# Performance work log

Measured on AMD Instinct MI355X. Metric: run time of the kernel, lower is better.

Reference implementation:

```python
import jax, jax.numpy as jnp
import numpy as np

B, T, C = 1, 2048, 2048
H, KH, HD = 16, 4, 128  # n_head, n_kv_head, head_dim
ROPE_BASE = 10000.0


def setup_inputs() -> dict:
    key = jax.random.key(0)
    ks = jax.random.split(key, 5)
    s = 0.02
    return {
        "x": jax.random.normal(ks[0], (B, T, C), jnp.float32),
        "Wq": jax.random.normal(ks[1], (C, H * HD), jnp.float32) * s,
        "Wk": jax.random.normal(ks[2], (C, KH * HD), jnp.float32) * s,
        "Wv": jax.random.normal(ks[3], (C, KH * HD), jnp.float32) * s,
        "Wo": jax.random.normal(ks[4], (H * HD, C), jnp.float32) * s,
        "position_ids": jnp.arange(T, dtype=jnp.int32),
    }


def _rotate_half(a):
    h = a.shape[-1] // 2
    return jnp.concatenate([-a[..., h:], a[..., :h]], axis=-1)


def reference(x, Wq, Wk, Wv, Wo, position_ids):
    b, t, c = x.shape
    n_rep = H // KH
    # projections -> [B, heads, T, HD]
    q = (x @ Wq).reshape(b, t, H, HD).transpose(0, 2, 1, 3)
    k = (x @ Wk).reshape(b, t, KH, HD).transpose(0, 2, 1, 3)
    v = (x @ Wv).reshape(b, t, KH, HD).transpose(0, 2, 1, 3)
    # rotary embedding cache [T, HD]
    inv_freq = 1.0 / (ROPE_BASE ** (jnp.arange(0, HD, 2, dtype=jnp.float32) / HD))
    pos = jnp.arange(t, dtype=jnp.float32)
    freqs = pos[:, None] * inv_freq[None, :]
    emb = jnp.concatenate([freqs, freqs], axis=-1)
    cos = jnp.cos(emb)[position_ids][None, None]  # [1,1,T,HD]
    sin = jnp.sin(emb)[position_ids][None, None]
    q = q * cos + _rotate_half(q) * sin
    k = k * cos + _rotate_half(k) * sin
    # GQA: group query heads instead of materializing repeated K/V
    qg = q.reshape(b, KH, n_rep, t, HD)
    scale = jnp.float32(1.0 / np.sqrt(HD))
    scores = jnp.einsum('bgrtd,bgsd->bgrts', qg, k) * scale
    causal = jnp.tril(jnp.ones((t, t), dtype=bool))
    scores = jnp.where(causal, scores, jnp.float32(-1e30))
    p = jax.nn.softmax(scores, axis=-1)
    y = jnp.einsum('bgrts,bgsd->bgrtd', p, v)
    y = y.reshape(b, H, t, HD).transpose(0, 2, 1, 3).reshape(b, t, H * HD)
    return y @ Wo
```

## Files before the change

kernel.cpp:

```cpp
#include <hip/hip_runtime.h>

typedef unsigned short u16;
using bf16x8 = __attribute__((ext_vector_type(8))) short;
using f32x4  = __attribute__((ext_vector_type(4))) float;

#define GLD16(g, l)                                                            \
  __builtin_amdgcn_global_load_lds(                                            \
      (const __attribute__((address_space(1))) void*)(g),                      \
      (__attribute__((address_space(3))) void*)(l), 16, 0, 0)

__device__ __forceinline__ u16 f2b(float x) {
  union { float f; unsigned u; } v; v.f = x;
  unsigned r = v.u + 0x7FFF + ((v.u >> 16) & 1);
  return (u16)(r >> 16);
}

__global__ void cast_bf16_kernel(const float* __restrict__ in,
                                 u16* __restrict__ out, int n4) {
  int i = blockIdx.x * blockDim.x + threadIdx.x;
  int stride = gridDim.x * blockDim.x;
  for (; i < n4; i += stride) {
    float4 v = ((const float4*)in)[i];
    ushort4 o;
    o.x = f2b(v.x); o.y = f2b(v.y); o.z = f2b(v.z); o.w = f2b(v.w);
    ((ushort4*)out)[i] = o;
  }
}

__global__ void transpose_w_kernel(const float* __restrict__ src,
                                   u16* __restrict__ dst, int K, int N) {
  __shared__ float tile[32][33];
  int n0 = blockIdx.x * 32, k0 = blockIdx.y * 32;
  int tx = threadIdx.x, ty = threadIdx.y;
#pragma unroll
  for (int r = 0; r < 4; r++)
    tile[ty + r * 8][tx] = src[(size_t)(k0 + ty + r * 8) * N + n0 + tx];
  __syncthreads();
#pragma unroll
  for (int r = 0; r < 4; r++)
    dst[(size_t)(n0 + ty + r * 8) * K + k0 + tx] = f2b(tile[tx][ty + r * 8]);
}

__global__ void transpose_v_kernel(const u16* __restrict__ src,
                                   u16* __restrict__ dst) {
  __shared__ u16 tile[32][33];
  int h = blockIdx.z;
  int t0 = blockIdx.x * 32, d0 = blockIdx.y * 32;
  const u16* s = src + (size_t)h * 2048 * 128;
  u16* d = dst + (size_t)h * 128 * 2048;
  int tx = threadIdx.x, ty = threadIdx.y;
#pragma unroll
  for (int r = 0; r < 4; r++)
    tile[ty + r * 8][tx] = s[(size_t)(t0 + ty + r * 8) * 128 + d0 + tx];
  __syncthreads();
#pragma unroll
  for (int r = 0; r < 4; r++)
    d[(size_t)(d0 + ty + r * 8) * 2048 + t0 + tx] = tile[tx][ty + r * 8];
}

__global__ __launch_bounds__(256, 2)
void gemm_bt_128(const u16* __restrict__ A, const u16* __restrict__ Bt,
                 float* __restrict__ C, int M, int N, int K) {
  __shared__ u16 As[128 * 32];
  __shared__ u16 Bs[128 * 32];
  const int tid = threadIdx.x;
  const int lane = tid & 63;
  const int w = tid >> 6;
  const int wr = w >> 1, wc = w & 1;
  const int m0 = blockIdx.y * 128, n0 = blockIdx.x * 128;

  f32x4 acc[4][4] = {};

  const int srow = tid >> 2, skg = tid & 3;
  const u16* Ag0 = A + (size_t)(m0 + srow) * K + skg * 8;
  const u16* Ag1 = A + (size_t)(m0 + 64 + srow) * K + skg * 8;
  const u16* Bg0 = Bt + (size_t)(n0 + srow) * K + skg * 8;
  const u16* Bg1 = Bt + (size_t)(n0 + 64 + srow) * K + skg * 8;
  u16* Al0 = As + tid * 8;
  u16* Al1 = As + (256 + tid) * 8;
  u16* Bl0 = Bs + tid * 8;
  u16* Bl1 = Bs + (256 + tid) * 8;

  const int frow = lane & 15, fk = (lane >> 4) * 8;

  for (int k0 = 0; k0 < K; k0 += 32) {
    GLD16(Ag0 + k0, Al0);
    GLD16(Ag1 + k0, Al1);
    GLD16(Bg0 + k0, Bl0);
    GLD16(Bg1 + k0, Bl1);
    __syncthreads();
    bf16x8 av[4], bv[4];
#pragma unroll
    for (int m = 0; m < 4; m++)
      av[m] = *(const bf16x8*)(As + (wr * 64 + m * 16 + frow) * 32 + fk);
#pragma unroll
    for (int n = 0; n < 4; n++)
      bv[n] = *(const bf16x8*)(Bs + (wc * 64 + n * 16 + frow) * 32 + fk);
#pragma unroll
    for (int m = 0; m < 4; m++)
#pragma unroll
      for (int n = 0; n < 4; n++)
        acc[m][n] =
            __builtin_amdgcn_mfma_f32_16x16x32_bf16(av[m], bv[n], acc[m][n], 0, 0, 0);
    __syncthreads();
  }

  const int crow = (lane >> 4) * 4, ccol = lane & 15;
#pragma unroll
  for (int m = 0; m < 4; m++)
#pragma unroll
    for (int n = 0; n < 4; n++)
#pragma unroll
      for (int r = 0; r < 4; r++)
        C[(size_t)(m0 + wr * 64 + m * 16 + crow + r) * N +
          (n0 + wc * 64 + n * 16 + ccol)] = acc[m][n][r];
}

__global__ void rope_kernel(const float* __restrict__ QKV,
                            const int* __restrict__ pos, u16* __restrict__ Qb,
                            u16* __restrict__ Kb, u16* __restrict__ Vb) {
  const int t = blockIdx.x, tid = threadIdx.x;
  const float p = (float)pos[t];
  const float* row = QKV + (size_t)t * 3072;
  const float qscale = 0.08838834764831845f;
  const float c0 = -0.015625f * 13.287712379549449f;
#pragma unroll
  for (int i = 0; i < 4; i++) {
    int idx = tid + i * 256;
    int head = idx >> 6, d = idx & 63;
    float inv = exp2f((float)d * c0);
    float ang = p * inv;
    float s = sinf(ang), c = cosf(ang);
    float a0 = row[head * 128 + d], a1 = row[head * 128 + d + 64];
    Qb[((size_t)head * 2048 + t) * 128 + d] = f2b((a0 * c - a1 * s) * qscale);
    Qb[((size_t)head * 2048 + t) * 128 + d + 64] = f2b((a1 * c + a0 * s) * qscale);
  }
  {
    int head = tid >> 6, d = tid & 63;
    float inv = exp2f((float)d * c0);
    float ang = p * inv;
    float s = sinf(ang), c = cosf(ang);
    float a0 = row[2048 + head * 128 + d], a1 = row[2048 + head * 128 + d + 64];
    Kb[((size_t)head * 2048 + t) * 128 + d] = f2b(a0 * c - a1 * s);
    Kb[((size_t)head * 2048 + t) * 128 + d + 64] = f2b(a1 * c + a0 * s);
  }
#pragma unroll
  for (int i = 0; i < 2; i++) {
    int e = tid + i * 256;
    int kh = e >> 7, d = e & 127;
    Vb[((size_t)kh * 2048 + t) * 128 + d] = f2b(row[2560 + e]);
  }
}

__global__ __launch_bounds__(256, 2)
void attn_kernel(const u16* __restrict__ Qb, const u16* __restrict__ Kb,
                 const u16* __restrict__ Vtb, u16* __restrict__ Y) {
  __shared__ u16 Ks[2][64 * 128];
  __shared__ u16 Vs[2][128 * 64];
  __shared__ u16 Ps[4][16 * 64];
  const int tid = threadIdx.x, lane = tid & 63, w = tid >> 6;
  const int h = blockIdx.y, g = h >> 2;
  const int q0 = blockIdx.x * 64;
  const int qw = q0 + w * 16;
  const int frow = lane & 15, fgrp = lane >> 4;

  const u16* Kg = Kb + (size_t)g * 2048 * 128;
  const u16* Vg = Vtb + (size_t)g * 128 * 2048;

  bf16x8 qf[4];
  const u16* Qrow = Qb + ((size_t)h * 2048 + (qw + frow)) * 128 + fgrp * 8;
#pragma unroll
  for (int kf = 0; kf < 4; kf++) qf[kf] = *(const bf16x8*)(Qrow + kf * 32);

  f32x4 o[8] = {};
  float mrow[4], lrow[4];
#pragma unroll
  for (int r = 0; r < 4; r++) { mrow[r] = -1e30f; lrow[r] = 0.f; }

  const int njt = q0 / 64 + 1;

#pragma unroll
  for (int i = 0; i < 4; i++) {
    int p = tid + i * 256;
    int kr = p >> 4, kc = (p & 15) ^ (kr & 7);
    GLD16(Kg + (size_t)kr * 128 + kc * 8, &Ks[0][p * 8]);
    int vr = p >> 3, vc = (p & 7) ^ (vr & 7);
    GLD16(Vg + (size_t)vr * 2048 + vc * 8, &Vs[0][p * 8]);
  }
  __syncthreads();

  for (int jt = 0; jt < njt; jt++) {
    const int buf = jt & 1;
    if (jt + 1 < njt) {
      const int j0n = (jt + 1) * 64;
#pragma unroll
      for (int i = 0; i < 4; i++) {
        int p = tid + i * 256;
        int kr = p >> 4, kc = (p & 15) ^ (kr & 7);
        GLD16(Kg + (size_t)(j0n + kr) * 128 + kc * 8, &Ks[buf ^ 1][p * 8]);
        int vr = p >> 3, vc = (p & 7) ^ (vr & 7);
        GLD16(Vg + (size_t)vr * 2048 + j0n + vc * 8, &Vs[buf ^ 1][p * 8]);
      }
    }
    f32x4 sc[4] = {};
#pragma unroll
    for (int c = 0; c < 4; c++)
#pragma unroll
      for (int kf = 0; kf < 4; kf++) {
        int row = c * 16 + frow;
        bf16x8 kv = *(const bf16x8*)(
            &Ks[buf][row * 128 + ((kf * 4 + fgrp) ^ (row & 7)) * 8]);
        sc[c] = __builtin_amdgcn_mfma_f32_16x16x32_bf16(qf[kf], kv, sc[c], 0, 0, 0);
      }
    if (jt == njt - 1) {
      const int j0 = jt * 64;
#pragma unroll
      for (int c = 0; c < 4; c++) {
        int j = j0 + c * 16 + frow;
#pragma unroll
        for (int r = 0; r < 4; r++)
          if (j > qw + fgrp * 4 + r) sc[c][r] = -1e30f;
      }
    }
    float pm[4];
#pragma unroll
    for (int r = 0; r < 4; r++)
      pm[r] = fmaxf(fmaxf(sc[0][r], sc[1][r]), fmaxf(sc[2][r], sc[3][r]));
#pragma unroll
    for (int off = 1; off < 16; off <<= 1)
#pragma unroll
      for (int r = 0; r < 4; r++) pm[r] = fmaxf(pm[r], __shfl_xor(pm[r], off, 64));
    float alpha[4], rs[4];
#pragma unroll
    for (int r = 0; r < 4; r++) {
      float mn = fmaxf(mrow[r], pm[r]);
      alpha[r] = __expf(mrow[r] - mn);
      mrow[r] = mn;
      float s = 0.f;
#pragma unroll
      for (int c = 0; c < 4; c++) { sc[c][r] = __expf(sc[c][r] - mn); s += sc[c][r]; }
      rs[r] = s;
    }
#pragma unroll
    for (int off = 1; off < 16; off <<= 1)
#pragma unroll
      for (int r = 0; r < 4; r++) rs[r] += __shfl_xor(rs[r], off, 64);
#pragma unroll
    for (int r = 0; r < 4; r++) lrow[r] = lrow[r] * alpha[r] + rs[r];
#pragma unroll
    for (int db = 0; db < 8; db++)
#pragma unroll
      for (int r = 0; r < 4; r++) o[db][r] *= alpha[r];
    u16* Pw = Ps[w];
#pragma unroll
    for (int c = 0; c < 4; c++)
#pragma unroll
      for (int r = 0; r < 4; r++) {
        int row = fgrp * 4 + r, col = c * 16 + frow;
        Pw[row * 64 + (((col >> 3) ^ row) & 7) * 8 + (col & 7)] = f2b(sc[c][r]);
      }
    asm volatile("s_waitcnt lgkmcnt(0)" ::: "memory");
    bf16x8 pf[2];
#pragma unroll
    for (int ks = 0; ks < 2; ks++)
      pf[ks] = *(const bf16x8*)(
          &Pw[frow * 64 + ((ks * 4 + fgrp) ^ (frow & 7)) * 8]);
#pragma unroll
    for (int db = 0; db < 8; db++)
#pragma unroll
      for (int ks = 0; ks < 2; ks++) {
        int row = db * 16 + frow;
        bf16x8 vf = *(const bf16x8*)(
            &Vs[buf][row * 64 + ((ks * 4 + fgrp) ^ (row & 7)) * 8]);
        o[db] = __builtin_amdgcn_mfma_f32_16x16x32_bf16(pf[ks], vf, o[db], 0, 0, 0);
      }
    __syncthreads();
  }
#pragma unroll
  for (int r = 0; r < 4; r++) {
    float inv = 1.0f / lrow[r];
    int t = qw + fgrp * 4 + r;
#pragma unroll
    for (int db = 0; db < 8; db++)
      Y[(size_t)t * 2048 + h * 128 + db * 16 + frow] = f2b(o[db][r] * inv);
  }
}

extern "C" void kernel_launch(void* const* d_in, const int* in_sizes, int n_in,
                              void* d_out, int out_size, void* d_ws,
                              size_t ws_size, hipStream_t stream) {
  const float* x  = (const float*)d_in[0];
  const float* Wq = (const float*)d_in[1];
  const float* Wk = (const float*)d_in[2];
  const float* Wv = (const float*)d_in[3];
  const float* Wo = (const float*)d_in[4];
  const int* pos  = (const int*)d_in[5];
  float* out = (float*)d_out;
  char* ws = (char*)d_ws;

  u16* xb      = (u16*)(ws + 0);
  u16* Wqkv_bt = (u16*)(ws + 8388608);
  u16* Wo_bt   = (u16*)(ws + 20971520);
  float* QKV   = (float*)(ws + 29360128);
  u16* Yb      = (u16*)(ws + 29360128);
  u16* Qb      = (u16*)(ws + 54525952);
  u16* Kb      = (u16*)(ws + 62914560);
  u16* Vb      = (u16*)(ws + 65011712);
  u16* Vtb     = (u16*)(ws + 67108864);

  cast_bf16_kernel<<<1024, 256, 0, stream>>>(x, xb, 2048 * 2048 / 4);
  transpose_w_kernel<<<dim3(64, 64), dim3(32, 8), 0, stream>>>(Wq, Wqkv_bt, 2048, 2048);
  transpose_w_kernel<<<dim3(16, 64), dim3(32, 8), 0, stream>>>(Wk, Wqkv_bt + (size_t)2048 * 2048, 2048, 512);
  transpose_w_kernel<<<dim3(16, 64), dim3(32, 8), 0, stream>>>(Wv, Wqkv_bt + (size_t)2560 * 2048, 2048, 512);
  transpose_w_kernel<<<dim3(64, 64), dim3(32, 8), 0, stream>>>(Wo, Wo_bt, 2048, 2048);

  gemm_bt_128<<<dim3(3072 / 128, 2048 / 128), 256, 0, stream>>>(xb, Wqkv_bt, QKV, 2048, 3072, 2048);

  rope_kernel<<<2048, 256, 0, stream>>>(QKV, pos, Qb, Kb, Vb);
  transpose_v_kernel<<<dim3(64, 4, 4), dim3(32, 8), 0, stream>>>(Vb, Vtb);

  attn_kernel<<<dim3(2048 / 64, 16), 256, 0, stream>>>(Qb, Kb, Vtb, Yb);

  gemm_bt_128<<<dim3(2048 / 128, 2048 / 128), 256, 0, stream>>>(Yb, Wo_bt, out, 2048, 2048, 2048);
}
```

Before: 285.1 us.

## Pair causal query tiles per block and skip rescale when max barely grows

Each attention block now handles two query tiles, t0 and 31-t0, back to back, so every block does the same 33 KV iterations. This balances the causal triangle and halves the grid to 16x16. The KV double-buffer prefetch carries across the seam between the two tiles. A lazy rescale also skips the alpha/exp correction of the output accumulators unless the running max rises by more than 8 in some row. That trades a bounded growth in exponent range for fewer multiplies per tile. Only 256 blocks now run, which may underfill the CUs.

```diff
diff --git a/kernel.cpp b/kernel.cpp
--- a/kernel.cpp
+++ b/kernel.cpp
@@ -160,48 +160,71 @@
   __shared__ u16 Ps[4][16 * 64];
   const int tid = threadIdx.x, lane = tid & 63, w = tid >> 6;
   const int h = blockIdx.y, g = h >> 2;
-  const int q0 = blockIdx.x * 64;
-  const int qw = q0 + w * 16;
   const int frow = lane & 15, fgrp = lane >> 4;
+  const int t0 = blockIdx.x;
+  const int t1 = 31 - t0;
+  const int n0p = t0 + 1;
 
   const u16* Kg = Kb + (size_t)g * 2048 * 128;
   const u16* Vg = Vtb + (size_t)g * 128 * 2048;
 
+#define STAGE(j0v, B)                                                          \
+  {                                                                            \
+    _Pragma("unroll")                                                          \
+    for (int i = 0; i < 4; i++) {                                              \
+      int p = tid + i * 256;                                                   \
+      int kr = p >> 4, kc = (p & 15) ^ (kr & 7);                               \
+      GLD16(Kg + (size_t)((j0v) + kr) * 128 + kc * 8, &Ks[B][p * 8]);          \
+      int vr = p >> 3, vc = (p & 7) ^ (vr & 7);                                \
+      GLD16(Vg + (size_t)vr * 2048 + (j0v) + vc * 8, &Vs[B][p * 8]);           \
+    }                                                                          \
+  }
+
+  int qw = t0 * 64 + w * 16;
   bf16x8 qf[4];
-  const u16* Qrow = Qb + ((size_t)h * 2048 + (qw + frow)) * 128 + fgrp * 8;
-#pragma unroll
-  for (int kf = 0; kf < 4; kf++) qf[kf] = *(const bf16x8*)(Qrow + kf * 32);
+  {
+    const u16* Qrow = Qb + ((size_t)h * 2048 + (qw + frow)) * 128 + fgrp * 8;
+#pragma unroll
+    for (int kf = 0; kf < 4; kf++) qf[kf] = *(const bf16x8*)(Qrow + kf * 32);
+  }
 
   f32x4 o[8] = {};
   float mrow[4], lrow[4];
 #pragma unroll
   for (int r = 0; r < 4; r++) { mrow[r] = -1e30f; lrow[r] = 0.f; }
 
-  const int njt = q0 / 64 + 1;
-
-#pragma unroll
-  for (int i = 0; i < 4; i++) {
-    int p = tid + i * 256;
-    int kr = p >> 4, kc = (p & 15) ^ (kr & 7);
-    GLD16(Kg + (size_t)kr * 128 + kc * 8, &Ks[0][p * 8]);
-    int vr = p >> 3, vc = (p & 7) ^ (vr & 7);
-    GLD16(Vg + (size_t)vr * 2048 + vc * 8, &Vs[0][p * 8]);
-  }
+  STAGE(0, 0);
   __syncthreads();
 
-  for (int jt = 0; jt < njt; jt++) {
-    const int buf = jt & 1;
-    if (jt + 1 < njt) {
-      const int j0n = (jt + 1) * 64;
-#pragma unroll
-      for (int i = 0; i < 4; i++) {
-        int p = tid + i * 256;
-        int kr = p >> 4, kc = (p & 15) ^ (kr & 7);
-        GLD16(Kg + (size_t)(j0n + kr) * 128 + kc * 8, &Ks[buf ^ 1][p * 8]);
-        int vr = p >> 3, vc = (p & 7) ^ (vr & 7);
-        GLD16(Vg + (size_t)vr * 2048 + j0n + vc * 8, &Vs[buf ^ 1][p * 8]);
-      }
-    }
+  for (int it = 0; it < 33; ++it) {
+    const int buf = it & 1;
+    if (it + 1 < 33) {
+      const int itn = it + 1;
+      const int jn = (itn < n0p) ? itn : itn - n0p;
+      STAGE(jn * 64, buf ^ 1);
+    }
+    if (it == n0p) {
+#pragma unroll
+      for (int r = 0; r < 4; r++) {
+        float inv = 1.0f / lrow[r];
+        int t = qw + fgrp * 4 + r;
+#pragma unroll
+        for (int db = 0; db < 8; db++)
+          Y[(size_t)t * 2048 + h * 128 + db * 16 + frow] = f2b(o[db][r] * inv);
+      }
+#pragma unroll
+      for (int db = 0; db < 8; db++)
+#pragma unroll
+        for (int r = 0; r < 4; r++) o[db][r] = 0.f;
+#pragma unroll
+      for (int r = 0; r < 4; r++) { mrow[r] = -1e30f; lrow[r] = 0.f; }
+      qw = t1 * 64 + w * 16;
+      const u16* Qrow = Qb + ((size_t)h * 2048 + (qw + frow)) * 128 + fgrp * 8;
+#pragma unroll
+      for (int kf = 0; kf < 4; kf++) qf[kf] = *(const bf16x8*)(Qrow + kf * 32);
+    }
+    const bool diag = (it == t0) || (it == 32);
+
     f32x4 sc[4] = {};
 #pragma unroll
     for (int c = 0; c < 4; c++)
@@ -212,14 +235,13 @@
             &Ks[buf][row * 128 + ((kf * 4 + fgrp) ^ (row & 7)) * 8]);
         sc[c] = __builtin_amdgcn_mfma_f32_16x16x32_bf16(qf[kf], kv, sc[c], 0, 0, 0);
       }
-    if (jt == njt - 1) {
-      const int j0 = jt * 64;
+    if (diag) {
 #pragma unroll
       for (int c = 0; c < 4; c++) {
-        int j = j0 + c * 16 + frow;
+        int j = c * 16 + frow;
 #pragma unroll
         for (int r = 0; r < 4; r++)
-          if (j > qw + fgrp * 4 + r) sc[c][r] = -1e30f;
+          if (j > (w * 16 + fgrp * 4 + r)) sc[c][r] = -1e30f;
       }
     }
     float pm[4];
@@ -230,15 +252,26 @@
     for (int off = 1; off < 16; off <<= 1)
 #pragma unroll
       for (int r = 0; r < 4; r++) pm[r] = fmaxf(pm[r], __shfl_xor(pm[r], off, 64));
-    float alpha[4], rs[4];
+    bool nd = false;
+#pragma unroll
+    for (int r = 0; r < 4; r++) nd = nd || (pm[r] > mrow[r] + 8.f);
+    if (__any(nd)) {
+#pragma unroll
+      for (int r = 0; r < 4; r++) {
+        float mn = fmaxf(mrow[r], pm[r]);
+        float alpha = __expf(mrow[r] - mn);
+        mrow[r] = mn;
+        lrow[r] *= alpha;
+#pragma unroll
+        for (int db = 0; db < 8; db++) o[db][r] *= alpha;
+      }
+    }
+    float rs[4];
 #pragma unroll
     for (int r = 0; r < 4; r++) {
-      float mn = fmaxf(mrow[r], pm[r]);
-      alpha[r] = __expf(mrow[r] - mn);
-      mrow[r] = mn;
       float s = 0.f;
 #pragma unroll
-      for (int c = 0; c < 4; c++) { sc[c][r] = __expf(sc[c][r] - mn); s += sc[c][r]; }
+      for (int c = 0; c < 4; c++) { sc[c][r] = __expf(sc[c][r] - mrow[r]); s += sc[c][r]; }
       rs[r] = s;
     }
 #pragma unroll
@@ -246,11 +279,7 @@
 #pragma unroll
       for (int r = 0; r < 4; r++) rs[r] += __shfl_xor(rs[r], off, 64);
 #pragma unroll
-    for (int r = 0; r < 4; r++) lrow[r] = lrow[r] * alpha[r] + rs[r];
-#pragma unroll
-    for (int db = 0; db < 8; db++)
-#pragma unroll
-      for (int r = 0; r < 4; r++) o[db][r] *= alpha[r];
+    for (int r = 0; r < 4; r++) lrow[r] += rs[r];
     u16* Pw = Ps[w];
 #pragma unroll
     for (int c = 0; c < 4; c++)
@@ -284,6 +313,7 @@
     for (int db = 0; db < 8; db++)
       Y[(size_t)t * 2048 + h * 128 + db * 16 + frow] = f2b(o[db][r] * inv);
   }
+#undef STAGE
 }
 
 extern "C" void kernel_launch(void* const* d_in, const int* in_sizes, int n_in,
@@ -319,7 +349,7 @@
   rope_kernel<<<2048, 256, 0, stream>>>(QKV, pos, Qb, Kb, Vb);
   transpose_v_kernel<<<dim3(64, 4, 4), dim3(32, 8), 0, stream>>>(Vb, Vtb);
 
-  attn_kernel<<<dim3(2048 / 64, 16), 256, 0, stream>>>(Qb, Kb, Vtb, Yb);
+  attn_kernel<<<dim3(16, 16), 256, 0, stream>>>(Qb, Kb, Vtb, Yb);
 
   gemm_bt_128<<<dim3(2048 / 128, 2048 / 128), 256, 0, stream>>>(Yb, Wo_bt, out, 2048, 2048, 2048);
 }
```

Result: faster. 271.0 us (-4.9%).
